# Kernel tuning notes

Measured on AMD Instinct MI355X. Metric: run time of the kernel, lower is better.

## Reference

```python
import jax, jax.numpy as jnp
import numpy as np

EPS = 1e-5      # BatchNorm eps (eval mode, running stats at init: mean=0, var=1)
SLOPE = 0.2     # LeakyReLU negative slope


def _knn_idx(x, k):
    # x: (B, N, D) -> (B, N, k) indices of k nearest neighbors (squared L2, feature space)
    sq = jnp.sum(x * x, axis=-1)                              # (B, N)
    dist = sq[:, :, None] + sq[:, None, :] - 2.0 * jnp.einsum('bnd,bmd->bnm', x, x)
    return jax.lax.top_k(-dist, k)[1]                         # nearest = largest of -dist


def _bn_lrelu(y, gamma, beta):
    # eval BatchNorm with running_mean=0, running_var=1, then LeakyReLU(0.2)
    y = y * (gamma / jnp.sqrt(1.0 + EPS)) + beta
    return jnp.where(y >= 0, y, SLOPE * y)


def _edge_conv(x, W, gamma, beta, k):
    # x: (B, N, D); W: (C_out, 2D). Returns (B, N, C_out) after max over k neighbors.
    idx = _knn_idx(x, k)                                      # (B, N, k)
    nb = jax.vmap(lambda xt, i: xt[i])(x, idx)                # (B, N, k, D) neighbor gather
    ctr = jnp.broadcast_to(x[:, :, None, :], nb.shape)
    feat = jnp.concatenate([nb - ctr, ctr], axis=-1)          # (B, N, k, 2D)
    y = jnp.einsum('bnkd,od->bnko', feat, W)                  # 1x1 conv (no bias)
    y = _bn_lrelu(y, gamma, beta)
    return jnp.max(y, axis=2)                                 # max-pool over neighbors


def setup_inputs() -> dict:
    key = jax.random.key(0)
    ks = jax.random.split(key, 16)
    B, N, k, out_dim = 8, 4096, 20, 512
    x = jax.random.normal(ks[0], (B, 3, N), dtype=jnp.float32)
    dims = [(64, 6), (64, 128), (128, 128), (256, 256), (out_dim, 512)]
    inp = {'x': x, 'k': k}
    for i, (co, ci) in enumerate(dims, start=1):
        inp[f'W{i}'] = jax.random.normal(ks[3 * i - 2], (co, ci), dtype=jnp.float32) * (1.0 / np.sqrt(ci))
        inp[f'g{i}'] = jax.random.uniform(ks[3 * i - 1], (co,), dtype=jnp.float32, minval=0.5, maxval=1.5)
        inp[f'b{i}'] = 0.1 * jax.random.normal(ks[3 * i], (co,), dtype=jnp.float32)
    return inp


def reference(x, W1, g1, b1, W2, g2, b2, W3, g3, b3, W4, g4, b4, W5, g5, b5, k):
    xt = jnp.transpose(x, (0, 2, 1))                          # (B, N, 3)
    x1 = _edge_conv(xt, W1, g1, b1, k)                        # (B, N, 64)
    x2 = _edge_conv(x1, W2, g2, b2, k)                        # (B, N, 64)
    x3 = _edge_conv(x2, W3, g3, b3, k)                        # (B, N, 128)
    x4 = _edge_conv(x3, W4, g4, b4, k)                        # (B, N, 256)
    h = jnp.concatenate([x1, x2, x3, x4], axis=-1)            # (B, N, 512)
    y = _bn_lrelu(jnp.einsum('bnd,od->bno', h, W5), g5, b5)   # (B, N, out_dim)
    return jnp.concatenate([jnp.max(y, axis=1), jnp.mean(y, axis=1)], axis=-1)  # (B, 2*out_dim)
```

## Files before the change

kernel.cpp:

```cpp
#include <hip/hip_runtime.h>
#include <math.h>

#define BATCH 8
#define N_PTS 4096
#define KNN 20
#define EPS_BN 1e-5f
#define SLOPE 0.2f
#define M_ROWS (BATCH * N_PTS)

typedef __attribute__((ext_vector_type(8))) short short8;
typedef __attribute__((ext_vector_type(4))) float float4v;
typedef __attribute__((ext_vector_type(16))) float float16v;

__device__ __forceinline__ unsigned short f2bf(float f) {
    unsigned u = __float_as_uint(f);
    unsigned r = (u + 0x7FFFu + ((u >> 16) & 1u)) >> 16;
    return (unsigned short)r;
}
__device__ __forceinline__ float bf2f(unsigned short h) {
    return __uint_as_float((unsigned)h << 16);
}

__global__ void convert_x1(const float* __restrict__ x,
                           unsigned short* __restrict__ xh, unsigned short* __restrict__ xl,
                           float* __restrict__ sq) {
    int i = blockIdx.x * blockDim.x + threadIdx.x;
    if (i >= M_ROWS) return;
    int b = i / N_PTS, n = i % N_PTS;
    float v[3], s = 0.f;
    #pragma unroll
    for (int d = 0; d < 3; ++d) {
        v[d] = x[((size_t)b * 3 + d) * N_PTS + n];
        s += v[d] * v[d];
    }
    sq[i] = s;
    #pragma unroll
    for (int d = 0; d < 32; ++d) {
        float f = (d < 3) ? v[d] : 0.f;
        unsigned short h = f2bf(f);
        xh[(size_t)i * 32 + d] = h;
        xl[(size_t)i * 32 + d] = f2bf(f - bf2f(h));
    }
}

__global__ void sqnorm_hl(const unsigned short* __restrict__ hh,
                          const unsigned short* __restrict__ hl,
                          int D, float* __restrict__ sq) {
    int w = threadIdx.x >> 6, lane = threadIdx.x & 63;
    int row = blockIdx.x * 4 + w;
    if (row >= M_ROWS) return;
    const unsigned short* ph = hh + (size_t)row * 512;
    const unsigned short* pl = hl + (size_t)row * 512;
    float s = 0.f;
    for (int d = lane; d < D; d += 64) {
        float v = bf2f(ph[d]) + bf2f(pl[d]);
        s += v * v;
    }
    #pragma unroll
    for (int off = 32; off > 0; off >>= 1) s += __shfl_down(s, off, 64);
    if (lane == 0) sq[row] = s;
}

__global__ void repack_edge_split(const float* __restrict__ W, int Co, int D, int KP,
                                  unsigned short* __restrict__ Wh, unsigned short* __restrict__ Wl) {
    int i = blockIdx.x * blockDim.x + threadIdx.x;
    int tot = 2 * Co * KP;
    if (i >= tot) return;
    int r = i / KP, d = i % KP;
    float v = 0.f;
    if (d < D) v = (r < Co) ? W[(size_t)r * 2 * D + d] : W[(size_t)(r - Co) * 2 * D + D + d];
    unsigned short h = f2bf(v);
    Wh[i] = h; Wl[i] = f2bf(v - bf2f(h));
}

__global__ void repack_w5_split(const float* __restrict__ W,
                                unsigned short* __restrict__ Wh, unsigned short* __restrict__ Wl) {
    int i = blockIdx.x * blockDim.x + threadIdx.x;
    if (i >= 512 * 512) return;
    float v = W[i];
    unsigned short h = f2bf(v);
    Wh[i] = h; Wl[i] = f2bf(v - bf2f(h));
}

template<int DPAD>
__launch_bounds__(256, 2)
__global__ void knn_mfma(const unsigned short* __restrict__ Xh,
                         const unsigned short* __restrict__ Xl,
                         int strideX,
                         const float* __restrict__ sq, int* __restrict__ idxout) {
    constexpr int KS16 = DPAD / 16;
    constexpr int C8   = DPAD / 8;
    constexpr int XK   = (C8 - 1) < 7 ? (C8 - 1) : 7;
    constexpr int SB   = 64 * DPAD;
    constexpr int NIT  = (64 * C8) / 256;
    constexpr size_t STAGE = (size_t)2 * SB * 2 + (size_t)64 * 65 * 4 + 64 * 4 + 256 * 4;
    constexpr size_t MERGE = (size_t)64 * 61 * 4 * 2;
    constexpr size_t POOL  = STAGE > MERGE ? STAGE : MERGE;
    __shared__ __align__(16) char smem[POOL];
    unsigned short* BhS = (unsigned short*)smem;
    unsigned short* BlS = BhS + SB;
    float* Sf  = (float*)(smem + (size_t)2 * SB * 2);
    float* sqs = Sf + 64 * 65;
    float* thrT = sqs + 64;
    float*    kb = (float*)smem;
    unsigned* ib = (unsigned*)(kb + 64 * 61);

    const int b = blockIdx.y;
    const int row0 = blockIdx.x * 64;
    const int tid = threadIdx.x;
    const int w = tid >> 6, lane = tid & 63;
    const int l31 = lane & 31, lh = lane >> 5;
    const int r = tid & 63, t = tid >> 6;
    const int rbase = (w & 1) * 32;
    const int cb32  = (w >> 1) * 32;

    const unsigned short* Xhb = Xh + (size_t)b * N_PTS * strideX;
    const unsigned short* Xlb = Xl + (size_t)b * N_PTS * strideX;
    const float* sqb = sq + (size_t)b * N_PTS;

    short8 ah[KS16], al[KS16];
    #pragma unroll
    for (int ks = 0; ks < KS16; ++ks) {
        size_t o = (size_t)(row0 + rbase + l31) * strideX + ks * 16 + lh * 8;
        ah[ks] = *(const short8*)(Xhb + o);
        al[ks] = *(const short8*)(Xlb + o);
    }

    float fv[KNN]; int fi[KNN];
    #pragma unroll
    for (int p = 0; p < KNN; ++p) { fv[p] = INFINITY; fi[p] = 0x7FFFFFFF; }

    #pragma unroll
    for (int it = 0; it < NIT; ++it) {
        int tt = tid + it * 256;
        int col = tt / C8, kcs = tt % C8;
        int kcg = kcs ^ (col & XK);
        size_t o = (size_t)col * strideX + kcg * 8;
        *(short8*)&BhS[tt * 8] = *(const short8*)(Xhb + o);
        *(short8*)&BlS[tt * 8] = *(const short8*)(Xlb + o);
    }
    if (tid < 64) sqs[tid] = sqb[tid];
    thrT[tid] = INFINITY;

    for (int c0 = 0; c0 < N_PTS; c0 += 64) {
        __syncthreads();

        float16v acc = {};

        const int colL = cb32 + l31;
        const int cbase_us = colL * DPAD;
        #pragma unroll
        for (int ks = 0; ks < KS16; ++ks) {
            int ch = ((ks * 2 + lh) ^ (colL & XK)) * 8;
            short8 bh = *(const short8*)&BhS[cbase_us + ch];
            short8 bl = *(const short8*)&BlS[cbase_us + ch];
            acc = __builtin_amdgcn_mfma_f32_32x32x16_bf16(ah[ks], bh, acc, 0, 0, 0);
            acc = __builtin_amdgcn_mfma_f32_32x32x16_bf16(al[ks], bh, acc, 0, 0, 0);
            acc = __builtin_amdgcn_mfma_f32_32x32x16_bf16(ah[ks], bl, acc, 0, 0, 0);
        }

        {
            float sc = sqs[colL];
            int pos = (colL & 3) * 16 + (colL >> 2);
            #pragma unroll
            for (int reg = 0; reg < 16; ++reg) {
                int rowL = rbase + (reg & 3) + 8 * (reg >> 2) + 4 * lh;
                Sf[rowL * 65 + pos] = sc - 2.f * acc[reg];
            }
        }
        __syncthreads();

        const int c1 = c0 + 64;
        short8 sh[NIT], sl[NIT];
        float sqv = 0.f;
        if (c1 < N_PTS) {
            #pragma unroll
            for (int it = 0; it < NIT; ++it) {
                int tt = tid + it * 256;
                int col = tt / C8, kcs = tt % C8;
                int kcg = kcs ^ (col & XK);
                size_t o = (size_t)(c1 + col) * strideX + kcg * 8;
                sh[it] = *(const short8*)(Xhb + o);
                sl[it] = *(const short8*)(Xlb + o);
            }
            if (tid < 64) sqv = sqb[c1 + tid];
        }

        float fT = fminf(fminf(thrT[r], thrT[64 + r]),
                         fminf(thrT[128 + r], thrT[192 + r]));

        const int sbase = r * 65 + t * 16;
        unsigned mask = 0;
        {
            float f19 = fv[KNN - 1];
            #pragma unroll
            for (int jj = 0; jj < 16; ++jj) {
                float v = Sf[sbase + jj];
                if (v < f19 && v <= fT) mask |= (1u << jj);
            }
        }
        while (mask) {
            int jj = __ffs(mask) - 1;
            mask &= mask - 1;
            float v = Sf[sbase + jj];
            if (v < fv[KNN - 1]) {
                fv[KNN - 1] = v;
                fi[KNN - 1] = c0 + (jj << 2) + t;
                #pragma unroll
                for (int p = KNN - 1; p > 0; --p) {
                    float va = fv[p - 1], vb = fv[p];
                    int   ia = fi[p - 1], ic = fi[p];
                    bool sw = vb < va;
                    fv[p - 1] = sw ? vb : va; fv[p] = sw ? va : vb;
                    fi[p - 1] = sw ? ic : ia; fi[p] = sw ? ia : ic;
                }
            }
        }

        if (c1 < N_PTS) {
            #pragma unroll
            for (int it = 0; it < NIT; ++it) {
                int tt = tid + it * 256;
                *(short8*)&BhS[tt * 8] = sh[it];
                *(short8*)&BlS[tt * 8] = sl[it];
            }
            if (tid < 64) sqs[tid] = sqv;
        }

        thrT[t * 64 + r] = fv[KNN - 1];
    }
    __syncthreads();

    if (t > 0) {
        #pragma unroll
        for (int p = 0; p < KNN; ++p) {
            kb[r * 61 + (t - 1) * KNN + p] = fv[p];
            ib[r * 61 + (t - 1) * KNN + p] = (unsigned)fi[p];
        }
    }
    __syncthreads();
    if (tid < 64) {
        #pragma unroll 1
        for (int qq = 0; qq < 3 * KNN; ++qq) {
            float    v  = kb[tid * 61 + qq];
            unsigned ii = ib[tid * 61 + qq];
            bool ins = (v < fv[KNN - 1]) ||
                       (v == fv[KNN - 1] && (int)ii < fi[KNN - 1]);
            if (ins) {
                fv[KNN - 1] = v; fi[KNN - 1] = (int)ii;
                #pragma unroll
                for (int p = KNN - 1; p > 0; --p) {
                    float va = fv[p - 1], vb = fv[p];
                    int   ia = fi[p - 1], ic = fi[p];
                    bool sw = (vb < va) || (vb == va && ic < ia);
                    fv[p - 1] = sw ? vb : va; fv[p] = sw ? va : vb;
                    fi[p - 1] = sw ? ic : ia; fi[p] = sw ? ia : ic;
                }
            }
        }
        int* op = idxout + ((size_t)(b * N_PTS + row0 + tid)) * KNN;
        #pragma unroll
        for (int p = 0; p < KNN; ++p) op[p] = fi[p];
    }
}

__launch_bounds__(256)
__global__ void fgemm(const unsigned short* __restrict__ Ah, const unsigned short* __restrict__ Al,
                      int strideA, int K,
                      const unsigned short* __restrict__ Wh, const unsigned short* __restrict__ Wl,
                      int C, float* __restrict__ out, int fuse_bn,
                      const float* __restrict__ g, const float* __restrict__ beta) {
    __shared__ unsigned short AhS[128 * 40];
    __shared__ unsigned short AlS[128 * 40];
    __shared__ unsigned short BhS[128 * 40];
    __shared__ unsigned short BlS[128 * 40];

    const int c0 = blockIdx.x * 128;
    const int m0 = blockIdx.y * 128;
    const int tid = threadIdx.x;
    const int w = tid >> 6, lane = tid & 63;
    const int n = lane & 15, q = lane >> 4;

    float4v acc[2][8];
    #pragma unroll
    for (int rt = 0; rt < 2; ++rt)
        #pragma unroll
        for (int ct = 0; ct < 8; ++ct) acc[rt][ct] = (float4v){0.f, 0.f, 0.f, 0.f};

    for (int kk = 0; kk < K; kk += 32) {
        __syncthreads();
        for (int tt = tid; tt < 512; tt += 256) {
            int rr = tt >> 2, c8 = tt & 3;
            size_t oa = (size_t)(m0 + rr) * strideA + kk + c8 * 8;
            *(short8*)&AhS[rr * 40 + c8 * 8] = *(const short8*)(Ah + oa);
            *(short8*)&AlS[rr * 40 + c8 * 8] = *(const short8*)(Al + oa);
            size_t ob = (size_t)(c0 + rr) * K + kk + c8 * 8;
            *(short8*)&BhS[rr * 40 + c8 * 8] = *(const short8*)(Wh + ob);
            *(short8*)&BlS[rr * 40 + c8 * 8] = *(const short8*)(Wl + ob);
        }
        __syncthreads();

        short8 af[2][2];
        #pragma unroll
        for (int rt = 0; rt < 2; ++rt) {
            af[rt][0] = *(const short8*)&AhS[(w * 32 + rt * 16 + n) * 40 + q * 8];
            af[rt][1] = *(const short8*)&AlS[(w * 32 + rt * 16 + n) * 40 + q * 8];
        }
        #pragma unroll
        for (int ct = 0; ct < 8; ++ct) {
            short8 bh = *(const short8*)&BhS[(ct * 16 + n) * 40 + q * 8];
            short8 bl = *(const short8*)&BlS[(ct * 16 + n) * 40 + q * 8];
            #pragma unroll
            for (int rt = 0; rt < 2; ++rt) {
                acc[rt][ct] = __builtin_amdgcn_mfma_f32_16x16x32_bf16(af[rt][0], bh, acc[rt][ct], 0, 0, 0);
                acc[rt][ct] = __builtin_amdgcn_mfma_f32_16x16x32_bf16(af[rt][1], bh, acc[rt][ct], 0, 0, 0);
                acc[rt][ct] = __builtin_amdgcn_mfma_f32_16x16x32_bf16(af[rt][0], bl, acc[rt][ct], 0, 0, 0);
            }
        }
    }

    #pragma unroll
    for (int rt = 0; rt < 2; ++rt)
        #pragma unroll
        for (int ct = 0; ct < 8; ++ct) {
            int c = c0 + ct * 16 + n;
            float sc = 1.f, bt = 0.f;
            if (fuse_bn) { sc = g[c] / sqrtf(1.f + EPS_BN); bt = beta[c]; }
            #pragma unroll
            for (int e = 0; e < 4; ++e) {
                int m = m0 + w * 32 + rt * 16 + q * 4 + e;
                float v = acc[rt][ct][e];
                if (fuse_bn) { v = v * sc + bt; v = (v >= 0.f) ? v : SLOPE * v; }
                out[(size_t)m * C + c] = v;
            }
        }
}

__global__ void pool_kernel(const float* __restrict__ zc2, int Co,
                            const int* __restrict__ idx,
                            const float* __restrict__ g, const float* __restrict__ beta,
                            unsigned short* __restrict__ hh, unsigned short* __restrict__ hl,
                            int hoff) {
    int n = blockIdx.x, b = blockIdx.y;
    int o = threadIdx.x;
    size_t bn = (size_t)b * N_PTS + n;
    const int* ip = idx + bn * KNN;
    float zn   = zc2[bn * (size_t)(2 * Co) + o];
    float base = zc2[bn * (size_t)(2 * Co) + Co + o] - zn;
    float m = -INFINITY;
    #pragma unroll
    for (int j = 0; j < KNN; ++j) {
        size_t rr = (size_t)b * N_PTS + ip[j];
        m = fmaxf(m, zc2[rr * (size_t)(2 * Co) + o]);
    }
    float y = m + base;
    float sc = g[o] / sqrtf(1.f + EPS_BN);
    y = y * sc + beta[o];
    y = (y >= 0.f) ? y : SLOPE * y;
    unsigned short h = f2bf(y);
    hh[bn * 512 + hoff + o] = h;
    hl[bn * 512 + hoff + o] = f2bf(y - bf2f(h));
}

__global__ void reduce_partial(const float* __restrict__ y5,
                               float* __restrict__ pmax, float* __restrict__ psum) {
    int chunk = blockIdx.x, b = blockIdx.y, c = threadIdx.x;
    float mx = -INFINITY, sm = 0.f;
    for (int qq = 0; qq < 128; ++qq) {
        int n = chunk * 128 + qq;
        float v = y5[((size_t)b * N_PTS + n) * 512 + c];
        mx = fmaxf(mx, v);
        sm += v;
    }
    pmax[((size_t)b * 32 + chunk) * 512 + c] = mx;
    psum[((size_t)b * 32 + chunk) * 512 + c] = sm;
}

__global__ void reduce_final(const float* __restrict__ pmax,
                             const float* __restrict__ psum,
                             float* __restrict__ out) {
    int i = blockIdx.x * blockDim.x + threadIdx.x;
    if (i >= BATCH * 512) return;
    int b = i / 512, c = i % 512;
    float mx = -INFINITY, sm = 0.f;
    for (int qq = 0; qq < 32; ++qq) {
        mx = fmaxf(mx, pmax[((size_t)b * 32 + qq) * 512 + c]);
        sm += psum[((size_t)b * 32 + qq) * 512 + c];
    }
    out[(size_t)b * 1024 + c] = mx;
    out[(size_t)b * 1024 + 512 + c] = sm * (1.f / 4096.f);
}

extern "C" void kernel_launch(void* const* d_in, const int* in_sizes, int n_in,
                              void* d_out, int out_size, void* d_ws, size_t ws_size,
                              hipStream_t stream) {
    const float* x = (const float*)d_in[0];
    const float* W[5], *gg[5], *bb[5];
    for (int i = 0; i < 5; ++i) {
        W[i]  = (const float*)d_in[2 + 3 * i];
        gg[i] = (const float*)d_in[3 + 3 * i];
        bb[i] = (const float*)d_in[4 + 3 * i];
    }
    float* outp = (float*)d_out;

    char* wsb = (char*)d_ws;
    size_t off = 0;
    unsigned short* x1h = (unsigned short*)(wsb + off); off += (size_t)M_ROWS * 32 * 2;
    unsigned short* x1l = (unsigned short*)(wsb + off); off += (size_t)M_ROWS * 32 * 2;
    float* sq = (float*)(wsb + off); off += (size_t)M_ROWS * 4;
    int*   idx = (int*)(wsb + off); off += (size_t)M_ROWS * KNN * 4;
    unsigned short* Wh = (unsigned short*)(wsb + off); off += (size_t)512 * 512 * 2;
    unsigned short* Wl = (unsigned short*)(wsb + off); off += (size_t)512 * 512 * 2;
    unsigned short* hh = (unsigned short*)(wsb + off); off += (size_t)M_ROWS * 512 * 2;
    unsigned short* hl = (unsigned short*)(wsb + off); off += (size_t)M_ROWS * 512 * 2;
    float* zc2 = (float*)(wsb + off); off += (size_t)M_ROWS * 512 * 4;
    float* pmx = (float*)(wsb + off); off += (size_t)BATCH * 32 * 512 * 4;
    float* psm = (float*)(wsb + off); off += (size_t)BATCH * 32 * 512 * 4;
    (void)ws_size; (void)in_sizes; (void)n_in; (void)out_size;

    convert_x1<<<(M_ROWS + 255) / 256, 256, 0, stream>>>(x, x1h, x1l, sq);

    struct L { int D, Co, KP, hoff; };
    const L layers[4] = { {3, 64, 32, 0}, {64, 64, 64, 64}, {64, 128, 64, 128}, {128, 256, 128, 256} };

    for (int li = 0; li < 4; ++li) {
        const L& ly = layers[li];
        const unsigned short* Ahp;
        const unsigned short* Alp;
        int strideA;
        if (li == 0) { Ahp = x1h; Alp = x1l; strideA = 32; }
        else {
            int po = layers[li - 1].hoff;
            Ahp = hh + po; Alp = hl + po; strideA = 512;
            sqnorm_hl<<<M_ROWS / 4, 256, 0, stream>>>(Ahp, Alp, ly.D, sq);
        }

        if (li == 0)
            knn_mfma<32><<<dim3(N_PTS / 64, BATCH), 256, 0, stream>>>(Ahp, Alp, strideA, sq, idx);
        else if (ly.D == 64)
            knn_mfma<64><<<dim3(N_PTS / 64, BATCH), 256, 0, stream>>>(Ahp, Alp, strideA, sq, idx);
        else
            knn_mfma<128><<<dim3(N_PTS / 64, BATCH), 256, 0, stream>>>(Ahp, Alp, strideA, sq, idx);

        repack_edge_split<<<(2 * ly.Co * ly.KP + 255) / 256, 256, 0, stream>>>(
            W[li], ly.Co, ly.D, ly.KP, Wh, Wl);
        fgemm<<<dim3((2 * ly.Co) / 128, M_ROWS / 128), 256, 0, stream>>>(
            Ahp, Alp, strideA, ly.KP, Wh, Wl, 2 * ly.Co, zc2, 0, nullptr, nullptr);
        pool_kernel<<<dim3(N_PTS, BATCH), ly.Co, 0, stream>>>(
            zc2, ly.Co, idx, gg[li], bb[li], hh, hl, ly.hoff);
    }

    repack_w5_split<<<(512 * 512 + 255) / 256, 256, 0, stream>>>(W[4], Wh, Wl);
    fgemm<<<dim3(4, M_ROWS / 128), 256, 0, stream>>>(
        hh, hl, 512, 512, Wh, Wl, 512, zc2, 1, gg[4], bb[4]);

    reduce_partial<<<dim3(32, BATCH), 512, 0, stream>>>(zc2, pmx, psm);
    reduce_final<<<(BATCH * 512 + 255) / 256, 256, 0, stream>>>(pmx, psm, outp);
}
```

Measured before the change: 1.543 ms.

## Stream KNN tiles directly into LDS with async global_load_lds and split MFMA accumulators

```diff
diff --git a/kernel.cpp b/kernel.cpp
--- a/kernel.cpp
+++ b/kernel.cpp
@@ -9,6 +9,7 @@
 #define M_ROWS (BATCH * N_PTS)
 
 typedef __attribute__((ext_vector_type(8))) short short8;
+typedef __attribute__((ext_vector_type(2))) float float2v;
 typedef __attribute__((ext_vector_type(4))) float float4v;
 typedef __attribute__((ext_vector_type(16))) float float16v;
 
@@ -20,6 +21,15 @@
 __device__ __forceinline__ float bf2f(unsigned short h) {
     return __uint_as_float((unsigned)h << 16);
 }
+
+#define GLOAD_LDS16(gp, lp)                                                               \
+    __builtin_amdgcn_global_load_lds(                                                     \
+        (const __attribute__((address_space(1))) unsigned int*)(const void*)(gp),         \
+        (__attribute__((address_space(3))) unsigned int*)(void*)(lp), 16, 0, 0)
+#define GLOAD_LDS4(gp, lp)                                                                \
+    __builtin_amdgcn_global_load_lds(                                                     \
+        (const __attribute__((address_space(1))) unsigned int*)(const void*)(gp),         \
+        (__attribute__((address_space(3))) unsigned int*)(void*)(lp), 4, 0, 0)
 
 __global__ void convert_x1(const float* __restrict__ x,
                            unsigned short* __restrict__ xh, unsigned short* __restrict__ xl,
@@ -90,17 +100,17 @@
                          const float* __restrict__ sq, int* __restrict__ idxout) {
     constexpr int KS16 = DPAD / 16;
     constexpr int C8   = DPAD / 8;
-    constexpr int XK   = (C8 - 1) < 7 ? (C8 - 1) : 7;
+    constexpr int XK   = (C8 - 1) < 15 ? (C8 - 1) : 15;
     constexpr int SB   = 64 * DPAD;
     constexpr int NIT  = (64 * C8) / 256;
-    constexpr size_t STAGE = (size_t)2 * SB * 2 + (size_t)64 * 65 * 4 + 64 * 4 + 256 * 4;
+    constexpr size_t STAGE = (size_t)2 * SB * 2 + (size_t)64 * 66 * 4 + 64 * 4 + 256 * 4;
     constexpr size_t MERGE = (size_t)64 * 61 * 4 * 2;
     constexpr size_t POOL  = STAGE > MERGE ? STAGE : MERGE;
     __shared__ __align__(16) char smem[POOL];
     unsigned short* BhS = (unsigned short*)smem;
     unsigned short* BlS = BhS + SB;
     float* Sf  = (float*)(smem + (size_t)2 * SB * 2);
-    float* sqs = Sf + 64 * 65;
+    float* sqs = Sf + 64 * 66;
     float* thrT = sqs + 64;
     float*    kb = (float*)smem;
     unsigned* ib = (unsigned*)(kb + 64 * 61);
@@ -136,16 +146,18 @@
         int col = tt / C8, kcs = tt % C8;
         int kcg = kcs ^ (col & XK);
         size_t o = (size_t)col * strideX + kcg * 8;
-        *(short8*)&BhS[tt * 8] = *(const short8*)(Xhb + o);
-        *(short8*)&BlS[tt * 8] = *(const short8*)(Xlb + o);
-    }
-    if (tid < 64) sqs[tid] = sqb[tid];
+        int tb = (it * 256 + (tid & ~63)) * 8;
+        GLOAD_LDS16(Xhb + o, BhS + tb);
+        GLOAD_LDS16(Xlb + o, BlS + tb);
+    }
+    if (w == 0) GLOAD_LDS4(sqb + lane, sqs);
     thrT[tid] = INFINITY;
 
     for (int c0 = 0; c0 < N_PTS; c0 += 64) {
+        asm volatile("s_waitcnt vmcnt(0)" ::: "memory");
         __syncthreads();
 
-        float16v acc = {};
+        float16v a0 = {}, a1 = {}, a2 = {};
 
         const int colL = cb32 + l31;
         const int cbase_us = colL * DPAD;
@@ -154,9 +166,9 @@
             int ch = ((ks * 2 + lh) ^ (colL & XK)) * 8;
             short8 bh = *(const short8*)&BhS[cbase_us + ch];
             short8 bl = *(const short8*)&BlS[cbase_us + ch];
-            acc = __builtin_amdgcn_mfma_f32_32x32x16_bf16(ah[ks], bh, acc, 0, 0, 0);
-            acc = __builtin_amdgcn_mfma_f32_32x32x16_bf16(al[ks], bh, acc, 0, 0, 0);
-            acc = __builtin_amdgcn_mfma_f32_32x32x16_bf16(ah[ks], bl, acc, 0, 0, 0);
+            a0 = __builtin_amdgcn_mfma_f32_32x32x16_bf16(ah[ks], bh, a0, 0, 0, 0);
+            a1 = __builtin_amdgcn_mfma_f32_32x32x16_bf16(al[ks], bh, a1, 0, 0, 0);
+            a2 = __builtin_amdgcn_mfma_f32_32x32x16_bf16(ah[ks], bl, a2, 0, 0, 0);
         }
 
         {
@@ -165,14 +177,12 @@
             #pragma unroll
             for (int reg = 0; reg < 16; ++reg) {
                 int rowL = rbase + (reg & 3) + 8 * (reg >> 2) + 4 * lh;
-                Sf[rowL * 65 + pos] = sc - 2.f * acc[reg];
+                Sf[rowL * 66 + pos] = sc - 2.f * (a0[reg] + a1[reg] + a2[reg]);
             }
         }
         __syncthreads();
 
         const int c1 = c0 + 64;
-        short8 sh[NIT], sl[NIT];
-        float sqv = 0.f;
         if (c1 < N_PTS) {
             #pragma unroll
             for (int it = 0; it < NIT; ++it) {
@@ -180,23 +190,27 @@
                 int col = tt / C8, kcs = tt % C8;
                 int kcg = kcs ^ (col & XK);
                 size_t o = (size_t)(c1 + col) * strideX + kcg * 8;
-                sh[it] = *(const short8*)(Xhb + o);
-                sl[it] = *(const short8*)(Xlb + o);
-            }
-            if (tid < 64) sqv = sqb[c1 + tid];
+                int tb = (it * 256 + (tid & ~63)) * 8;
+                GLOAD_LDS16(Xhb + o, BhS + tb);
+                GLOAD_LDS16(Xlb + o, BlS + tb);
+            }
+            if (w == 0) GLOAD_LDS4(sqb + c1 + lane, sqs);
         }
 
         float fT = fminf(fminf(thrT[r], thrT[64 + r]),
                          fminf(thrT[128 + r], thrT[192 + r]));
 
-        const int sbase = r * 65 + t * 16;
+        const int sbase = r * 66 + t * 16;
         unsigned mask = 0;
         {
             float f19 = fv[KNN - 1];
-            #pragma unroll
-            for (int jj = 0; jj < 16; ++jj) {
-                float v = Sf[sbase + jj];
-                if (v < f19 && v <= fT) mask |= (1u << jj);
+            float2v c2[8];
+            #pragma unroll
+            for (int u = 0; u < 8; ++u) c2[u] = *(const float2v*)&Sf[sbase + 2 * u];
+            #pragma unroll
+            for (int u = 0; u < 8; ++u) {
+                if (c2[u][0] < f19 && c2[u][0] <= fT) mask |= (1u << (2 * u));
+                if (c2[u][1] < f19 && c2[u][1] <= fT) mask |= (1u << (2 * u + 1));
             }
         }
         while (mask) {
@@ -215,16 +229,6 @@
                     fi[p - 1] = sw ? ic : ia; fi[p] = sw ? ia : ic;
                 }
             }
-        }
-
-        if (c1 < N_PTS) {
-            #pragma unroll
-            for (int it = 0; it < NIT; ++it) {
-                int tt = tid + it * 256;
-                *(short8*)&BhS[tt * 8] = sh[it];
-                *(short8*)&BlS[tt * 8] = sl[it];
-            }
-            if (tid < 64) sqs[tid] = sqv;
         }
 
         thrT[t * 64 + r] = fv[KNN - 1];
```

New measurement: 1.605 ms. +4.0%, slower.
